# Performance work log

Hardware: AMD Instinct MI355X
Metric: run time of the kernel (lower is better)

The kernel has to match this reference:

```python
import jax, jax.numpy as jnp
import numpy as np

B, S, E = 2, 2048, 2048
H, KVH = 16, 4
D = E // H            # 128
N_REP = H // KVH      # 4


def setup_inputs() -> dict:
    key = jax.random.key(0)
    ks = jax.random.split(key, 5)
    x = jax.random.normal(ks[0], (B, S, E), dtype=jnp.float32)
    # kaiming-normal-ish linear weights, torch layout [out_features, in_features]
    wq_w = jax.random.normal(ks[1], (H * D, E), dtype=jnp.float32) * (2.0 / E) ** 0.5
    wk_w = jax.random.normal(ks[2], (KVH * D, E), dtype=jnp.float32) * (2.0 / E) ** 0.5
    wv_w = jax.random.normal(ks[3], (KVH * D, E), dtype=jnp.float32) * (2.0 / E) ** 0.5
    wo_w = jax.random.normal(ks[4], (E, E), dtype=jnp.float32) * (2.0 / E) ** 0.5
    # standard RoPE frequencies: theta = 10000
    inv_freq = 1.0 / (10000.0 ** (np.arange(0, D, 2, dtype=np.float32) / D))  # [D/2]
    t = np.arange(S, dtype=np.float32)
    ang = np.outer(t, inv_freq)  # [S, D/2]
    freqs_cos = jnp.asarray(np.cos(ang), dtype=jnp.float32)
    freqs_sin = jnp.asarray(np.sin(ang), dtype=jnp.float32)
    return {"x": x, "wq_w": wq_w, "wk_w": wk_w, "wv_w": wv_w, "wo_w": wo_w,
            "freqs_cos": freqs_cos, "freqs_sin": freqs_sin, "start_pos": 0}


def _rope(t, cos, sin):
    # t: [B, S, h, D]; cos/sin: [S, D/2] -> complex multiply on (even, odd) pairs
    tr = t.reshape(*t.shape[:-1], -1, 2)
    xr, xi = tr[..., 0], tr[..., 1]
    c = cos[None, :, None, :]
    s = sin[None, :, None, :]
    orr = xr * c - xi * s
    oi = xr * s + xi * c
    return jnp.stack([orr, oi], axis=-1).reshape(t.shape)


def reference(x, wq_w, wk_w, wv_w, wo_w, freqs_cos, freqs_sin, start_pos):
    b, s, e = x.shape
    q = jnp.einsum('bse,fe->bsf', x, wq_w).reshape(b, s, H, D)
    k = jnp.einsum('bse,fe->bsf', x, wk_w).reshape(b, s, KVH, D)
    v = jnp.einsum('bse,fe->bsf', x, wv_w).reshape(b, s, KVH, D)
    q = _rope(q, freqs_cos, freqs_sin)
    k = _rope(k, freqs_cos, freqs_sin)
    # faithful to torch .repeat(1,1,n_rep,1): TILE kv heads -> head h uses kv head h % KVH
    k = jnp.tile(k, (1, 1, N_REP, 1))  # [b, s, H, D]
    v = jnp.tile(v, (1, 1, N_REP, 1))
    q = q.transpose(0, 2, 1, 3)  # [b, H, s, D]
    k = k.transpose(0, 2, 1, 3)
    v = v.transpose(0, 2, 1, 3)
    scores = jnp.einsum('bhqd,bhkd->bhqk', q, k) * (1.0 / D ** 0.5)
    causal = jnp.tril(jnp.ones((s, s), dtype=bool))
    scores = jnp.where(causal[None, None], scores, -jnp.inf)
    attn = jax.nn.softmax(scores, axis=-1)
    out = jnp.einsum('bhqk,bhkd->bhqd', attn, v)
    out = out.transpose(0, 2, 1, 3).reshape(b, s, e)
    return jnp.einsum('bse,fe->bsf', out, wo_w)
```

## Files before the change

kernel.cpp:

```cpp
#include <hip/hip_runtime.h>
#include <hip/hip_bf16.h>

typedef unsigned short u16;
typedef unsigned int u32;
typedef short bf16x8 __attribute__((ext_vector_type(8)));
typedef float f32x4 __attribute__((ext_vector_type(4)));

#define MFMA_BF16 __builtin_amdgcn_mfma_f32_16x16x32_bf16

#define B_   2
#define S_   2048
#define E_   2048
#define H_   16
#define KVH_ 4
#define D_   128
#define M_   (B_ * S_)
#define NQKV 3072
#define SCALE_ 0.08838834764831845f

__device__ __forceinline__ float b2f(u16 u) {
    union { u32 i; float f; } x; x.i = ((u32)u) << 16; return x.f;
}
__device__ __forceinline__ u16 f2b(float f) {
    __hip_bfloat16 h = __float2bfloat16(f);
    return *reinterpret_cast<u16*>(&h);
}

__device__ __forceinline__ void async16(const u16* g, u16* l) {
    __builtin_amdgcn_global_load_lds(
        (const __attribute__((address_space(1))) void*)g,
        (__attribute__((address_space(3))) void*)l, 16, 0, 0);
}

__device__ __forceinline__ uint4 pack8(const float* p) {
    float4 a = *reinterpret_cast<const float4*>(p);
    float4 b = *reinterpret_cast<const float4*>(p + 4);
    union { uint4 v; u16 h[8]; } pk;
    pk.h[0] = f2b(a.x); pk.h[1] = f2b(a.y); pk.h[2] = f2b(a.z); pk.h[3] = f2b(a.w);
    pk.h[4] = f2b(b.x); pk.h[5] = f2b(b.y); pk.h[6] = f2b(b.z); pk.h[7] = f2b(b.w);
    return pk.v;
}

__global__ __launch_bounds__(256)
void conv4(const float* __restrict__ s0, u16* __restrict__ d0, int n0,
           const float* __restrict__ s1, u16* __restrict__ d1, int n1,
           const float* __restrict__ s2, u16* __restrict__ d2, int n2,
           const float* __restrict__ s3, u16* __restrict__ d3) {
    int bid = blockIdx.x;
    const float* s; u16* d; size_t base;
    if (bid < n0)                { s = s0; d = d0; base = (size_t)bid * 2048; }
    else if (bid < n0 + n1)      { s = s1; d = d1; base = (size_t)(bid - n0) * 2048; }
    else if (bid < n0 + n1 + n2) { s = s2; d = d2; base = (size_t)(bid - n0 - n1) * 2048; }
    else                         { s = s3; d = d3; base = (size_t)(bid - n0 - n1 - n2) * 2048; }
    size_t i = base + (size_t)threadIdx.x * 8;
    *reinterpret_cast<uint4*>(d + i) = pack8(s + i);
}

template <int BN>
__device__ __forceinline__ void gemm_core(const u16* __restrict__ Ag,
                                          const u16* __restrict__ Bg,
                                          u16* lds, int m0,
                                          f32x4 (&acc)[8][BN / 64]) {
    constexpr int NREP  = BN / 64;
    constexpr int BUFSZ = 16384 + BN * 64;
    constexpr int BJ    = BN / 128;
    const int tid = threadIdx.x, wave = tid >> 6, lane = tid & 63;
    const int l15 = lane & 15, quad = lane >> 4;
    const int wm = wave & 1, wn = wave >> 1;

    const f32x4 zero4 = {0.f, 0.f, 0.f, 0.f};
    #pragma unroll
    for (int i = 0; i < 8; ++i)
        #pragma unroll
        for (int j = 0; j < NREP; ++j) acc[i][j] = zero4;

    auto stageA = [&](int p, int kt, int kb) {
        #pragma unroll
        for (int j = 0; j < 2; ++j) {
            const int rb = wave * 2 + j;
            async16(Ag + (size_t)(m0 + rb * 16 + l15) * E_ + kt + kb * 32 + quad * 8,
                    &lds[p * BUFSZ + (((rb << 1) | kb) << 9)]);
        }
    };
    auto stageB = [&](int p, int kt, int kb) {
        #pragma unroll
        for (int j = 0; j < BJ; ++j) {
            const int rb = wave * BJ + j;
            async16(Bg + (size_t)(rb * 16 + l15) * E_ + kt + kb * 32 + quad * 8,
                    &lds[p * BUFSZ + 16384 + (((rb << 1) | kb) << 9)]);
        }
    };
    auto sync_keepN = [&]() {
        if constexpr (BN == 256) asm volatile("s_waitcnt vmcnt(4)" ::: "memory");
        else                     asm volatile("s_waitcnt vmcnt(3)" ::: "memory");
        __builtin_amdgcn_sched_barrier(0);
        __builtin_amdgcn_s_barrier();
        __builtin_amdgcn_sched_barrier(0);
    };
    auto sync_drain = [&]() {
        asm volatile("s_waitcnt vmcnt(0)" ::: "memory");
        __builtin_amdgcn_sched_barrier(0);
        __builtin_amdgcn_s_barrier();
        __builtin_amdgcn_sched_barrier(0);
    };

    auto half = [&](int p, int kb, bool stage, int ktn) {
        bf16x8 bfr[NREP];
        #pragma unroll
        for (int ni = 0; ni < NREP; ++ni)
            bfr[ni] = *reinterpret_cast<const bf16x8*>(
                &lds[p * BUFSZ + 16384 + ((((wn * NREP + ni) << 1) | kb) << 9) + lane * 8]);
        if (stage) stageA(p ^ 1, ktn, kb);
        bf16x8 af[4];
        #pragma unroll
        for (int i = 0; i < 4; ++i)
            af[i] = *reinterpret_cast<const bf16x8*>(
                &lds[p * BUFSZ + ((((wm * 8 + i) << 1) | kb) << 9) + lane * 8]);
        __builtin_amdgcn_s_setprio(1);
        #pragma unroll
        for (int mi = 0; mi < 4; ++mi)
            #pragma unroll
            for (int ni = 0; ni < NREP; ++ni)
                acc[mi][ni] = MFMA_BF16(af[mi], bfr[ni], acc[mi][ni], 0, 0, 0);
        __builtin_amdgcn_s_setprio(0);
        if (stage) stageB(p ^ 1, ktn, kb);
        #pragma unroll
        for (int i = 0; i < 4; ++i)
            af[i] = *reinterpret_cast<const bf16x8*>(
                &lds[p * BUFSZ + ((((wm * 8 + 4 + i) << 1) | kb) << 9) + lane * 8]);
        __builtin_amdgcn_s_setprio(1);
        #pragma unroll
        for (int mi = 0; mi < 4; ++mi)
            #pragma unroll
            for (int ni = 0; ni < NREP; ++ni)
                acc[4 + mi][ni] = MFMA_BF16(af[mi], bfr[ni], acc[4 + mi][ni], 0, 0, 0);
        __builtin_amdgcn_s_setprio(0);
    };

    stageA(0, 0, 0); stageB(0, 0, 0);
    stageA(0, 0, 1); stageB(0, 0, 1);
    sync_keepN();

    int p = 0;
    for (int kt = 0; kt < E_ - 64; kt += 64) {
        half(p, 0, true, kt + 64);
        sync_keepN();
        half(p, 1, true, kt + 64);
        sync_keepN();
        p ^= 1;
    }
    half(p, 0, false, 0);
    sync_drain();
    half(p, 1, false, 0);
}

__global__ __launch_bounds__(512, 2)
void qkv_rope_gemm(const u16* __restrict__ xb, const u16* __restrict__ wqb,
                   const u16* __restrict__ wkb, const u16* __restrict__ wvb,
                   const float* __restrict__ fc, const float* __restrict__ fs,
                   u16* __restrict__ Qr, u16* __restrict__ Kr,
                   u16* __restrict__ Vr) {
    __shared__ __align__(16) u16 lds[2 * (16384 + 256 * 64)];
    const int m0 = blockIdx.y * 256, n0 = blockIdx.x * 256;

    const u16* wsel;
    if (n0 < 2048)      wsel = wqb + (size_t)n0 * E_;
    else if (n0 < 2560) wsel = wkb + (size_t)(n0 - 2048) * E_;
    else                wsel = wvb + (size_t)(n0 - 2560) * E_;

    f32x4 acc[8][4];
    gemm_core<256>(xb, wsel, lds, m0, acc);

    const int tid = threadIdx.x, wave = tid >> 6, lane = tid & 63;
    const int l15 = lane & 15, quad = lane >> 4;
    const int wm = wave & 1, wn = wave >> 1;
    const int mb_ = m0 + wm * 128, nbase = n0 + wn * 64;
    #pragma unroll
    for (int mi = 0; mi < 8; ++mi)
        #pragma unroll
        for (int ni = 0; ni < 4; ++ni)
            #pragma unroll
            for (int r = 0; r < 4; ++r) {
                int m = mb_ + mi * 16 + quad * 4 + r;
                int n = nbase + ni * 16 + l15;
                int b = m >> 11, s = m & 2047;
                float v = acc[mi][ni][r];
                float other = __shfl_xor(v, 1);
                if (n < 2560) {
                    int d = n & 127;
                    int fi = s * 64 + (d >> 1);
                    float c  = fc[fi];
                    float sn = fs[fi];
                    v = (n & 1) ? (other * sn + v * c) : (v * c - other * sn);
                }
                if (n < 2048) {
                    Qr[((size_t)(b * H_ + (n >> 7)) * S_ + s) * D_ + (n & 127)] = f2b(v);
                } else if (n < 2560) {
                    int kh = (n - 2048) >> 7;
                    Kr[((size_t)(b * KVH_ + kh) * S_ + s) * D_ + (n & 127)] = f2b(v);
                } else {
                    int kh = (n - 2560) >> 7;
                    Vr[((size_t)(b * KVH_ + kh) * S_ + s) * D_ + (n & 127)] = f2b(v);
                }
            }
}

__global__ __launch_bounds__(256)
void transpose_v(const u16* __restrict__ Vr, u16* __restrict__ VrT) {
    __shared__ u16 t[64][72];
    const int tid = threadIdx.x;
    const int s0 = blockIdx.x * 64, d0 = blockIdx.y * 64, g = blockIdx.z;
    const u16* src = Vr + (size_t)g * S_ * D_;
    u16* dst = VrT + (size_t)g * D_ * S_;
    #pragma unroll
    for (int i = 0; i < 2; ++i) {
        int c = tid + i * 256;
        int r = c >> 3, cc = (c & 7) * 8;
        *reinterpret_cast<uint4*>(&t[r][cc]) =
            *reinterpret_cast<const uint4*>(src + (size_t)(s0 + r) * D_ + d0 + cc);
    }
    __syncthreads();
    #pragma unroll
    for (int i = 0; i < 2; ++i) {
        int c = tid + i * 256;
        int r = c >> 3, cc = (c & 7) * 8;
        u16 tmp[8];
        #pragma unroll
        for (int e = 0; e < 8; ++e) tmp[e] = t[cc + e][r];
        *reinterpret_cast<uint4*>(dst + (size_t)(d0 + r) * S_ + s0 + cc) =
            *reinterpret_cast<const uint4*>(tmp);
    }
}

__global__ __launch_bounds__(512, 4)
void flash2(const u16* __restrict__ Qr, const u16* __restrict__ Kr,
            const u16* __restrict__ VrT, u16* __restrict__ AO) {
    __shared__ __align__(16) u16 Ks[128 * 128];
    __shared__ __align__(16) u16 Vs[128 * 128];
    const int tid = threadIdx.x, wave = tid >> 6, lane = tid & 63;
    const int l15 = lane & 15, quad = lane >> 4;
    const int qt = blockIdx.x, h = blockIdx.y, b = blockIdx.z;
    const int kvh = h & 3;
    const u16* Qb = Qr + (size_t)(b * H_ + h) * S_ * D_;
    const u16* Kb = Kr + (size_t)(b * KVH_ + kvh) * S_ * D_;
    const u16* Vb = VrT + (size_t)(b * KVH_ + kvh) * D_ * S_;
    const int q0 = qt * 128 + wave * 16;
    const int qg = q0 + l15;

    bf16x8 bq[4];
    #pragma unroll
    for (int kk = 0; kk < 4; ++kk)
        bq[kk] = *reinterpret_cast<const bf16x8*>(
            Qb + (size_t)qg * D_ + kk * 32 + quad * 8);

    f32x4 o[8];
    const f32x4 zero4 = {0.f, 0.f, 0.f, 0.f};
    #pragma unroll
    for (int i = 0; i < 8; ++i) o[i] = zero4;
    float m_i = -__builtin_inff(), l_i = 0.f;

    const u16* kp[4]; const u16* vp[4];
    #pragma unroll
    for (int jj = 0; jj < 4; ++jj) {
        int t = wave * 4 + jj;
        kp[jj] = Kb + (size_t)((t >> 2) * 16 + l15) * D_ + (t & 3) * 32 + quad * 8;
        vp[jj] = Vb + (size_t)((t >> 2) * 16 + l15) * S_ + (t & 3) * 32 + quad * 8;
    }

    const int ntiles = qt + 1;
    for (int j = 0; j < ntiles; ++j) {
        __syncthreads();
        #pragma unroll
        for (int jj = 0; jj < 4; ++jj) {
            int t = wave * 4 + jj;
            async16(kp[jj], &Ks[t * 512]);
            async16(vp[jj], &Vs[t * 512]);
        }
        __syncthreads();

        #pragma unroll
        for (int h2 = 0; h2 < 2; ++h2) {
            const int kvbase = j * 128 + h2 * 64;
            if (q0 + 15 < kvbase) continue;

            f32x4 st[4];
            #pragma unroll
            for (int kb = 0; kb < 4; ++kb) st[kb] = zero4;
            #pragma unroll
            for (int kk = 0; kk < 4; ++kk)
                #pragma unroll
                for (int kb = 0; kb < 4; ++kb) {
                    bf16x8 ak = *reinterpret_cast<const bf16x8*>(
                        &Ks[(((h2 * 4 + kb) << 2) | kk) * 512 + lane * 8]);
                    st[kb] = MFMA_BF16(ak, bq[kk], st[kb], 0, 0, 0);
                }

            float mx = -__builtin_inff();
            if (j == qt) {
                #pragma unroll
                for (int kb = 0; kb < 4; ++kb)
                    #pragma unroll
                    for (int r = 0; r < 4; ++r) {
                        float s = st[kb][r] * SCALE_;
                        if (kvbase + kb * 16 + quad * 4 + r > qg)
                            s = -__builtin_inff();
                        st[kb][r] = s;
                        mx = fmaxf(mx, s);
                    }
            } else {
                #pragma unroll
                for (int kb = 0; kb < 4; ++kb)
                    #pragma unroll
                    for (int r = 0; r < 4; ++r) {
                        float s = st[kb][r] * SCALE_;
                        st[kb][r] = s;
                        mx = fmaxf(mx, s);
                    }
            }
            mx = fmaxf(mx, __shfl_xor(mx, 16));
            mx = fmaxf(mx, __shfl_xor(mx, 32));
            float mnew = fmaxf(m_i, mx);
            float a = __expf(m_i - mnew);
            float sum = 0.f;
            #pragma unroll
            for (int kb = 0; kb < 4; ++kb)
                #pragma unroll
                for (int r = 0; r < 4; ++r) {
                    float p = __expf(st[kb][r] - mnew);
                    st[kb][r] = p;
                    sum += p;
                }
            sum += __shfl_xor(sum, 16);
            sum += __shfl_xor(sum, 32);
            l_i = l_i * a + sum;
            m_i = mnew;
            #pragma unroll
            for (int mi = 0; mi < 8; ++mi)
                #pragma unroll
                for (int r = 0; r < 4; ++r) o[mi][r] *= a;

            #pragma unroll
            for (int kf = 0; kf < 2; ++kf) {
                u32 pk[4];
                #pragma unroll
                for (int r = 0; r < 4; ++r)
                    pk[r] = (u32)f2b(st[kf * 2 + 0][r]) |
                            ((u32)f2b(st[kf * 2 + 1][r]) << 16);
                bf16x8 bp;
                u16* bh = (u16*)&bp;
                #pragma unroll
                for (int j2 = 0; j2 < 8; ++j2) {
                    int src = ((quad & 1) * 2 + (j2 >> 2)) * 16 + l15;
                    u32 v = __shfl((int)pk[j2 & 3], src);
                    bh[j2] = (lane >= 32) ? (u16)(v >> 16) : (u16)v;
                }
                #pragma unroll
                for (int mi = 0; mi < 8; ++mi) {
                    bf16x8 av = *reinterpret_cast<const bf16x8*>(
                        &Vs[(((mi << 2) | (h2 * 2 + kf)) * 512) + lane * 8]);
                    o[mi] = MFMA_BF16(av, bp, o[mi], 0, 0, 0);
                }
            }
        }
        #pragma unroll
        for (int jj = 0; jj < 4; ++jj) { kp[jj] += 128 * D_; vp[jj] += 128; }
    }

    float inv = 1.0f / l_i;
    size_t base = ((size_t)(b * S_ + qg)) * E_ + h * D_;
    #pragma unroll
    for (int mi = 0; mi < 8; ++mi) {
        u16 w[4];
        #pragma unroll
        for (int r = 0; r < 4; ++r) w[r] = f2b(o[mi][r] * inv);
        *reinterpret_cast<uint2*>(AO + base + mi * 16 + quad * 4) =
            *reinterpret_cast<const uint2*>(w);
    }
}

__global__ __launch_bounds__(512, 2)
void out_proj_gemm(const u16* __restrict__ ao, const u16* __restrict__ wob,
                   float* __restrict__ out) {
    __shared__ __align__(16) u16 lds[2 * (16384 + 128 * 64)];
    const int m0 = blockIdx.y * 256, n0 = blockIdx.x * 128;

    f32x4 acc[8][2];
    gemm_core<128>(ao, wob + (size_t)n0 * E_, lds, m0, acc);

    const int tid = threadIdx.x, wave = tid >> 6, lane = tid & 63;
    const int l15 = lane & 15, quad = lane >> 4;
    const int wm = wave & 1, wn = wave >> 1;
    const int mb_ = m0 + wm * 128, nbase = n0 + wn * 32;
    #pragma unroll
    for (int mi = 0; mi < 8; ++mi)
        #pragma unroll
        for (int ni = 0; ni < 2; ++ni)
            #pragma unroll
            for (int r = 0; r < 4; ++r) {
                int m = mb_ + mi * 16 + quad * 4 + r;
                int n = nbase + ni * 16 + l15;
                out[(size_t)m * E_ + n] = acc[mi][ni][r];
            }
}

extern "C" void kernel_launch(void* const* d_in, const int* in_sizes, int n_in,
                              void* d_out, int out_size, void* d_ws, size_t ws_size,
                              hipStream_t stream) {
    const float* x  = (const float*)d_in[0];
    const float* wq = (const float*)d_in[1];
    const float* wk = (const float*)d_in[2];
    const float* wv = (const float*)d_in[3];
    const float* wo = (const float*)d_in[4];
    const float* fc = (const float*)d_in[5];
    const float* fs = (const float*)d_in[6];
    float* out = (float*)d_out;

    u16* wqb = (u16*)d_ws;
    u16* xb  = wqb + 4194304;
    u16* Qr  = wqb + 12582912;
    u16* Kr  = wqb + 20971520;
    u16* Vr  = wqb + 23068672;
    u16* VrT = wqb;
    u16* wob = wqb;
    u16* AO  = xb;
    u16* wkb = (u16*)d_out;
    u16* wvb = wkb + 1048576;

    conv4<<<7168, 256, 0, stream>>>(x, xb, 4096, wq, wqb, 2048,
                                    wk, wkb, 512, wv, wvb);
    qkv_rope_gemm<<<dim3(NQKV / 256, M_ / 256), 512, 0, stream>>>(
        xb, wqb, wkb, wvb, fc, fs, Qr, Kr, Vr);
    transpose_v<<<dim3(S_ / 64, D_ / 64, B_ * KVH_), 256, 0, stream>>>(Vr, VrT);
    flash2<<<dim3(S_ / 128, H_, B_), 512, 0, stream>>>(Qr, Kr, VrT, AO);
    conv4<<<2048, 256, 0, stream>>>(wo, wob, 2048, nullptr, nullptr, 0,
                                    nullptr, nullptr, 0, nullptr, nullptr);
    out_proj_gemm<<<dim3(E_ / 128, M_ / 256), 512, 0, stream>>>(AO, wob, out);
}
```

Measured before the change: 388.1 us.

## Double-buffer 64-key K/V tiles in flash attention with deferred rescale and reversed scheduling

Splits the K/V tile into 64-key halves and double-buffers them in shared memory, so the async load of the next tile overlaps compute on the current one, using raw barriers and vmcnt waits. Launches the longest causal query tiles first by reversing the block index. Skips the running-max update and output rescale when the new max exceeds the old by at most 8, which lowers exp and multiply work but lets unnormalized values grow up to e^8. Adds s_setprio around the MFMA sections.

```diff
diff --git a/kernel.cpp b/kernel.cpp
--- a/kernel.cpp
+++ b/kernel.cpp
@@ -235,11 +235,12 @@
 __global__ __launch_bounds__(512, 4)
 void flash2(const u16* __restrict__ Qr, const u16* __restrict__ Kr,
             const u16* __restrict__ VrT, u16* __restrict__ AO) {
-    __shared__ __align__(16) u16 Ks[128 * 128];
-    __shared__ __align__(16) u16 Vs[128 * 128];
+    __shared__ __align__(16) u16 Ks[2][8192];
+    __shared__ __align__(16) u16 Vs[2][8192];
     const int tid = threadIdx.x, wave = tid >> 6, lane = tid & 63;
     const int l15 = lane & 15, quad = lane >> 4;
-    const int qt = blockIdx.x, h = blockIdx.y, b = blockIdx.z;
+    const int qt = gridDim.x - 1 - blockIdx.x;
+    const int h = blockIdx.y, b = blockIdx.z;
     const int kvh = h & 3;
     const u16* Qb = Qr + (size_t)(b * H_ + h) * S_ * D_;
     const u16* Kb = Kr + (size_t)(b * KVH_ + kvh) * S_ * D_;
@@ -259,44 +260,54 @@
     for (int i = 0; i < 8; ++i) o[i] = zero4;
     float m_i = -__builtin_inff(), l_i = 0.f;
 
-    const u16* kp[4]; const u16* vp[4];
-    #pragma unroll
-    for (int jj = 0; jj < 4; ++jj) {
-        int t = wave * 4 + jj;
-        kp[jj] = Kb + (size_t)((t >> 2) * 16 + l15) * D_ + (t & 3) * 32 + quad * 8;
-        vp[jj] = Vb + (size_t)((t >> 2) * 16 + l15) * S_ + (t & 3) * 32 + quad * 8;
-    }
-
-    const int ntiles = qt + 1;
-    for (int j = 0; j < ntiles; ++j) {
-        __syncthreads();
-        #pragma unroll
-        for (int jj = 0; jj < 4; ++jj) {
-            int t = wave * 4 + jj;
-            async16(kp[jj], &Ks[t * 512]);
-            async16(vp[jj], &Vs[t * 512]);
+    const int f0 = wave * 2, f1 = wave * 2 + 1;
+    const u16* kp0 = Kb + (size_t)((f0 >> 2) * 16 + l15) * D_ + (f0 & 3) * 32 + quad * 8;
+    const u16* kp1 = Kb + (size_t)((f1 >> 2) * 16 + l15) * D_ + (f1 & 3) * 32 + quad * 8;
+    const u16* vp0 = Vb + (size_t)((f0 >> 1) * 16 + l15) * S_ + (f0 & 1) * 32 + quad * 8;
+    const u16* vp1 = Vb + (size_t)((f1 >> 1) * 16 + l15) * S_ + (f1 & 1) * 32 + quad * 8;
+
+    const int nt = 2 * qt + 2;
+    async16(kp0, &Ks[0][f0 * 512]);
+    async16(kp1, &Ks[0][f1 * 512]);
+    async16(vp0, &Vs[0][f0 * 512]);
+    async16(vp1, &Vs[0][f1 * 512]);
+
+    int p = 0;
+    for (int t = 0; t < nt; ++t) {
+        __builtin_amdgcn_s_barrier();
+        if (t + 1 < nt) {
+            size_t ko = (size_t)(t + 1) * 64 * D_;
+            size_t vo = (size_t)(t + 1) * 64;
+            async16(kp0 + ko, &Ks[p ^ 1][f0 * 512]);
+            async16(kp1 + ko, &Ks[p ^ 1][f1 * 512]);
+            async16(vp0 + vo, &Vs[p ^ 1][f0 * 512]);
+            async16(vp1 + vo, &Vs[p ^ 1][f1 * 512]);
+            asm volatile("s_waitcnt vmcnt(4)" ::: "memory");
+        } else {
+            asm volatile("s_waitcnt vmcnt(0)" ::: "memory");
         }
-        __syncthreads();
-
-        #pragma unroll
-        for (int h2 = 0; h2 < 2; ++h2) {
-            const int kvbase = j * 128 + h2 * 64;
-            if (q0 + 15 < kvbase) continue;
-
+        __builtin_amdgcn_sched_barrier(0);
+        __builtin_amdgcn_s_barrier();
+        __builtin_amdgcn_sched_barrier(0);
+
+        const int kvbase = t * 64;
+        if (q0 + 15 >= kvbase) {
             f32x4 st[4];
             #pragma unroll
             for (int kb = 0; kb < 4; ++kb) st[kb] = zero4;
+            __builtin_amdgcn_s_setprio(1);
             #pragma unroll
             for (int kk = 0; kk < 4; ++kk)
                 #pragma unroll
                 for (int kb = 0; kb < 4; ++kb) {
                     bf16x8 ak = *reinterpret_cast<const bf16x8*>(
-                        &Ks[(((h2 * 4 + kb) << 2) | kk) * 512 + lane * 8]);
+                        &Ks[p][(((kb << 2) | kk) << 9) + lane * 8]);
                     st[kb] = MFMA_BF16(ak, bq[kk], st[kb], 0, 0, 0);
                 }
+            __builtin_amdgcn_s_setprio(0);
 
             float mx = -__builtin_inff();
-            if (j == qt) {
+            if (kvbase + 63 > q0) {
                 #pragma unroll
                 for (int kb = 0; kb < 4; ++kb)
                     #pragma unroll
@@ -319,25 +330,28 @@
             }
             mx = fmaxf(mx, __shfl_xor(mx, 16));
             mx = fmaxf(mx, __shfl_xor(mx, 32));
-            float mnew = fmaxf(m_i, mx);
+            const bool nodefer = !__all(mx - m_i <= 8.0f);
+            float mnew = nodefer ? fmaxf(m_i, mx) : m_i;
             float a = __expf(m_i - mnew);
             float sum = 0.f;
             #pragma unroll
             for (int kb = 0; kb < 4; ++kb)
                 #pragma unroll
                 for (int r = 0; r < 4; ++r) {
-                    float p = __expf(st[kb][r] - mnew);
-                    st[kb][r] = p;
-                    sum += p;
+                    float pv = __expf(st[kb][r] - mnew);
+                    st[kb][r] = pv;
+                    sum += pv;
                 }
             sum += __shfl_xor(sum, 16);
             sum += __shfl_xor(sum, 32);
             l_i = l_i * a + sum;
             m_i = mnew;
-            #pragma unroll
-            for (int mi = 0; mi < 8; ++mi)
-                #pragma unroll
-                for (int r = 0; r < 4; ++r) o[mi][r] *= a;
+            if (nodefer) {
+                #pragma unroll
+                for (int mi = 0; mi < 8; ++mi)
+                    #pragma unroll
+                    for (int r = 0; r < 4; ++r) o[mi][r] *= a;
+            }
 
             #pragma unroll
             for (int kf = 0; kf < 2; ++kf) {
@@ -354,16 +368,17 @@
                     u32 v = __shfl((int)pk[j2 & 3], src);
                     bh[j2] = (lane >= 32) ? (u16)(v >> 16) : (u16)v;
                 }
+                __builtin_amdgcn_s_setprio(1);
                 #pragma unroll
                 for (int mi = 0; mi < 8; ++mi) {
                     bf16x8 av = *reinterpret_cast<const bf16x8*>(
-                        &Vs[(((mi << 2) | (h2 * 2 + kf)) * 512) + lane * 8]);
+                        &Vs[p][(((mi << 1) | kf) << 9) + lane * 8]);
                     o[mi] = MFMA_BF16(av, bp, o[mi], 0, 0, 0);
                 }
+                __builtin_amdgcn_s_setprio(0);
             }
         }
-        #pragma unroll
-        for (int jj = 0; jj < 4; ++jj) { kp[jj] += 128 * D_; vp[jj] += 128; }
+        p ^= 1;
     }
 
     float inv = 1.0f / l_i;
```

New measurement: 380.3 us. 2.0% less time.
